# Optimization experiments

Hardware: AMD Instinct MI355X
Metric: run time of the kernel (lower is better)

## Reference

```python
import jax, jax.numpy as jnp
import numpy as np

DIM = 2048
N_HEADS = 16
N_KV_HEADS = 4
HEAD_DIM = DIM // N_HEADS


def setup_inputs() -> dict:
    key = jax.random.key(0)
    k1, k2, k3, k4, k5 = jax.random.split(key, 5)
    B, T = 2, 2048
    scale = 1.0 / np.sqrt(DIM)
    x = jax.random.normal(k1, (B, T, DIM), dtype=jnp.float32)
    # weights stored as [in, out] so forward is x @ W (same math as nn.Linear)
    Wq = jax.random.normal(k2, (DIM, DIM), dtype=jnp.float32) * scale
    Wk = jax.random.normal(k3, (DIM, N_KV_HEADS * HEAD_DIM), dtype=jnp.float32) * scale
    Wv = jax.random.normal(k4, (DIM, N_KV_HEADS * HEAD_DIM), dtype=jnp.float32) * scale
    Wo = jax.random.normal(k5, (DIM, DIM), dtype=jnp.float32) * scale
    return {"x": x, "Wq": Wq, "Wk": Wk, "Wv": Wv, "Wo": Wo}


def reference(x, Wq, Wk, Wv, Wo):
    B, T, C = x.shape
    G = N_HEADS // N_KV_HEADS  # query heads per kv head
    # projections
    q = (x @ Wq).reshape(B, T, N_KV_HEADS, G, HEAD_DIM)   # [B,T,K,G,d]
    k = (x @ Wk).reshape(B, T, N_KV_HEADS, HEAD_DIM)      # [B,T,K,d]
    v = (x @ Wv).reshape(B, T, N_KV_HEADS, HEAD_DIM)      # [B,T,K,d]
    # attention scores: grouped heads share kv head (no repeat_interleave copy)
    att = jnp.einsum('btkgd,bskd->bkgts', q, k) / np.sqrt(HEAD_DIM)  # [B,K,G,T,T]
    att = jax.nn.softmax(att, axis=-1)
    out = jnp.einsum('bkgts,bskd->btkgd', att, v).reshape(B, T, C)
    return out @ Wo
```

## Files before the change

kernel.cpp:

```cpp
#include <hip/hip_runtime.h>
#include <hip/hip_bf16.h>

typedef __hip_bfloat16 bf16;
typedef __attribute__((ext_vector_type(8))) short short8;
typedef __attribute__((ext_vector_type(4))) short short4v;
typedef __attribute__((ext_vector_type(4))) float f32x4;

#define DIMC 2048
#define TSEQ 2048
#define NB 2
#define KVH 4
#define NH 16
#define HD 128
#define KVD 512
#define QSCALE 0.12751744f

#if __has_builtin(__builtin_amdgcn_exp2f)
#define EXP2(x) __builtin_amdgcn_exp2f(x)
#else
#define EXP2(x) exp2f(x)
#endif

__device__ __forceinline__ void mfma16(f32x4& acc, short8 a, short8 b) {
  acc = __builtin_amdgcn_mfma_f32_16x16x32_bf16(a, b, acc, 0, 0, 0);
}

__device__ __forceinline__ void gload_lds16(const bf16* g, bf16* l) {
  __builtin_amdgcn_global_load_lds(
      (const __attribute__((address_space(1))) void*)g,
      (__attribute__((address_space(3))) void*)l, 16, 0, 0);
}

__device__ __forceinline__ int swz(int row, int col) {
  return col ^ ((row & 7) << 3);
}

__global__ __launch_bounds__(256) void f2b(const float* __restrict__ in,
                                           bf16* __restrict__ out, long n4) {
  long i = (long)blockIdx.x * 256 + threadIdx.x;
  if (i >= n4) return;
  const f32x4 v = *(const f32x4*)(in + i * 4);
  union { short4v s; bf16 h[4]; } u;
#pragma unroll
  for (int j = 0; j < 4; ++j) u.h[j] = __float2bfloat16(v[j]);
  *(short4v*)(out + i * 4) = u.s;
}

__global__ __launch_bounds__(256) void transpose_all(const float* __restrict__ Wq,
                                                     const float* __restrict__ Wk,
                                                     const float* __restrict__ Wv,
                                                     const float* __restrict__ Wo,
                                                     bf16* __restrict__ WT3,
                                                     bf16* __restrict__ WoT) {
  __shared__ bf16 tile[64][72];
  const int y = blockIdx.y;
  const float* in;
  bf16* out;
  int C, rb, cb;
  float scale = 1.0f;
  if (y < 32) {
    in = Wq; out = WT3; C = 2048;
    rb = y * 64; cb = blockIdx.x * 64; scale = QSCALE;
  } else if (y < 40) {
    in = Wk; out = WT3 + (long)2048 * DIMC; C = 512;
    rb = blockIdx.x * 64; cb = (y - 32) * 64;
  } else if (y < 48) {
    in = Wv; out = WT3 + (long)2560 * DIMC; C = 512;
    rb = blockIdx.x * 64; cb = (y - 40) * 64;
  } else {
    in = Wo; out = WoT; C = 2048;
    rb = (y - 48) * 64; cb = blockIdx.x * 64;
  }
  int tx = threadIdx.x & 63, ty = threadIdx.x >> 6;
  for (int i = ty; i < 64; i += 4)
    tile[i][tx] = __float2bfloat16(in[(long)(rb + i) * C + cb + tx] * scale);
  __syncthreads();
  for (int i = ty; i < 64; i += 4)
    out[(long)(cb + i) * DIMC + rb + tx] = tile[tx][i];
}

#define GEMM_BODY(A_, Bt_, K_)                                                  \
  const int tid = threadIdx.x;                                                  \
  const int lane = tid & 63, wid = tid >> 6;                                    \
  const long m0 = blockIdx.y * 128, n0 = blockIdx.x * 128;                      \
  const int wm = (wid >> 1) * 64, wn = (wid & 1) * 64;                          \
  f32x4 acc[4][4] = {};                                                         \
  const int srow = lane >> 2, scol = (lane & 3) * 8;                            \
  const bf16* Ag = A_ + (m0 + srow) * (long)K_ + scol;                          \
  const bf16* Bg = Bt_ + (n0 + srow) * (long)K_ + scol;                         \
  for (int k0 = 0; k0 < K_; k0 += 32) {                                         \
    for (int p = 0; p < 2; ++p) {                                               \
      int rr = p * 64 + wid * 16;                                               \
      gload_lds16(Ag + (long)rr * K_ + k0, As + rr * 32);                       \
      gload_lds16(Bg + (long)rr * K_ + k0, Bs + rr * 32);                       \
    }                                                                           \
    __syncthreads();                                                            \
    const int ko = (lane >> 4) * 8;                                             \
    short8 af[4], bq[4];                                                        \
    _Pragma("unroll") for (int i = 0; i < 4; ++i) {                             \
      af[i] = *(const short8*)(As + (wm + i * 16 + (lane & 15)) * 32 + ko);     \
      bq[i] = *(const short8*)(Bs + (wn + i * 16 + (lane & 15)) * 32 + ko);     \
    }                                                                           \
    _Pragma("unroll") for (int i = 0; i < 4; ++i)                               \
      _Pragma("unroll") for (int j = 0; j < 4; ++j)                             \
        mfma16(acc[i][j], af[i], bq[j]);                                        \
    __syncthreads();                                                            \
  }                                                                             \
  const int cr = (lane >> 4) * 4, cc = lane & 15;

__global__ __launch_bounds__(256) void gemm_qkv(const bf16* __restrict__ A,
                                                const bf16* __restrict__ Bt,
                                                bf16* __restrict__ qp,
                                                bf16* __restrict__ kp,
                                                bf16* __restrict__ vT) {
  __shared__ bf16 As[128 * 32];
  __shared__ bf16 Bs[128 * 32];
  GEMM_BODY(A, Bt, 2048)
#pragma unroll
  for (int i = 0; i < 4; ++i)
#pragma unroll
    for (int j = 0; j < 4; ++j)
#pragma unroll
      for (int r = 0; r < 4; ++r) {
        long m = m0 + wm + i * 16 + cr + r;
        long n = n0 + wn + j * 16 + cc;
        float val = acc[i][j][r];
        if (n0 < 2048) {
          qp[m * DIMC + n] = __float2bfloat16(val);
        } else if (n0 < 2560) {
          kp[m * KVD + (n - 2048)] = __float2bfloat16(val);
        } else {
          long nn = n - 2560;
          long z = (m >> 11) * 4 + (nn >> 7);
          vT[z * (HD * (long)TSEQ) + (nn & 127) * (long)TSEQ + (m & 2047)] =
              __float2bfloat16(val);
        }
      }
}

__global__ __launch_bounds__(256) void gemm_out(const bf16* __restrict__ A,
                                                const bf16* __restrict__ Bt,
                                                float* __restrict__ C) {
  __shared__ bf16 As[128 * 32];
  __shared__ bf16 Bs[128 * 32];
  GEMM_BODY(A, Bt, 2048)
#pragma unroll
  for (int i = 0; i < 4; ++i)
#pragma unroll
    for (int j = 0; j < 4; ++j)
#pragma unroll
      for (int r = 0; r < 4; ++r) {
        long m = m0 + wm + i * 16 + cr + r;
        long n = n0 + wn + j * 16 + cc;
        C[m * DIMC + n] = acc[i][j][r];
      }
}

__global__ __launch_bounds__(256, 2) void attn_fwd(const bf16* __restrict__ Qp,
                                                   const bf16* __restrict__ Kp,
                                                   const bf16* __restrict__ Vt,
                                                   bf16* __restrict__ op2,
                                                   float* __restrict__ mlb) {
  __shared__ bf16 Ks[2][32 * 128];
  __shared__ bf16 Vts[2][128 * 32];
  const int tid = threadIdx.x;
  const int lane = tid & 63, wid = tid >> 6;
  const int h = blockIdx.y;
  const int z = blockIdx.z;
  const int b = z & 1, half = z >> 1;
  const int s_lo = half * 1024, s_hi = s_lo + 1024;
  const int kv = h >> 2;
  const int t0 = blockIdx.x * 128;
  const int lr = lane & 15, lg = lane >> 4;

  short8 aq[2][4];
#pragma unroll
  for (int f = 0; f < 2; ++f) {
    const bf16* qrow =
        Qp + ((long)(b * TSEQ + t0 + wid * 32 + f * 16 + lr)) * DIMC + h * HD + lg * 8;
#pragma unroll
    for (int c = 0; c < 4; ++c) aq[f][c] = *(const short8*)(qrow + c * 32);
  }
  f32x4 o[2][8] = {};
  float mrun[2] = {-1e30f, -1e30f}, lrun[2] = {0.f, 0.f};

  const bf16* Kg = Kp + (long)b * TSEQ * KVD + kv * HD;
  const bf16* Vg = Vt + ((long)(b * KVH + kv)) * HD * TSEQ;

  const int krow = tid >> 3, kc0 = (tid & 7) * 16;
  const int vrow = tid >> 1, va = tid & 1;
  short8 kreg[2], vreg[2];
#pragma unroll
  for (int p = 0; p < 2; ++p) {
    kreg[p] = *(const short8*)(Kg + (long)(s_lo + krow) * KVD + kc0 + p * 8);
    vreg[p] = *(const short8*)(Vg + (long)vrow * TSEQ + s_lo + va * 16 + 8 * p);
  }

  for (int s0 = s_lo; s0 < s_hi; s0 += 32) {
    const int buf = (s0 >> 5) & 1;
    bf16* Kb = Ks[buf];
    bf16* Vb = Vts[buf];
#pragma unroll
    for (int p = 0; p < 2; ++p) {
      *(short8*)(Kb + krow * 128 + swz(krow, kc0 + p * 8)) = kreg[p];
      union { short8 v8; short4v q[2]; } u;
      u.v8 = vreg[p];
      int q1 = (2 * p + vrow) & 3, q2 = (2 * p + 1 + vrow) & 3;
      *(short4v*)(Vb + vrow * 32 + q1 * 8 + va * 4) = u.q[0];
      *(short4v*)(Vb + vrow * 32 + q2 * 8 + va * 4) = u.q[1];
    }
    __syncthreads();
    if (s0 + 32 < s_hi) {
#pragma unroll
      for (int p = 0; p < 2; ++p) {
        kreg[p] = *(const short8*)(Kg + (long)(s0 + 32 + krow) * KVD + kc0 + p * 8);
        vreg[p] = *(const short8*)(Vg + (long)vrow * TSEQ + s0 + 32 + va * 16 + 8 * p);
      }
    }

    f32x4 sacc[2][2] = {};
    __builtin_amdgcn_s_setprio(1);
#pragma unroll
    for (int sf = 0; sf < 2; ++sf)
#pragma unroll
      for (int c = 0; c < 4; ++c) {
        int row = sf * 16 + lr;
        short8 kf = *(const short8*)(Kb + row * 128 + swz(row, c * 32 + lg * 8));
        mfma16(sacc[0][sf], kf, aq[0][c]);
        mfma16(sacc[1][sf], kf, aq[1][c]);
      }
    __builtin_amdgcn_s_setprio(0);

    union { short8 s; bf16 h[8]; } pb[2];
#pragma unroll
    for (int f = 0; f < 2; ++f) {
      float tmax = sacc[f][0][0];
#pragma unroll
      for (int sf = 0; sf < 2; ++sf)
#pragma unroll
        for (int r = 0; r < 4; ++r) tmax = fmaxf(tmax, sacc[f][sf][r]);
      tmax = fmaxf(tmax, __shfl_xor(tmax, 16));
      tmax = fmaxf(tmax, __shfl_xor(tmax, 32));
      if (__any(tmax > mrun[f] + 8.0f)) {
        float mnew = fmaxf(mrun[f], tmax);
        float fac = EXP2(mrun[f] - mnew);
        mrun[f] = mnew;
        lrun[f] *= fac;
#pragma unroll
        for (int df = 0; df < 8; ++df) o[f][df] *= fac;
      }
      float ps = 0.f;
#pragma unroll
      for (int r = 0; r < 4; ++r) {
        float v0 = EXP2(sacc[f][0][r] - mrun[f]);
        float v1 = EXP2(sacc[f][1][r] - mrun[f]);
        ps += v0 + v1;
        pb[f].h[r] = __float2bfloat16(v0);
        pb[f].h[4 + r] = __float2bfloat16(v1);
      }
      ps += __shfl_xor(ps, 16);
      ps += __shfl_xor(ps, 32);
      lrun[f] += ps;
    }

    __builtin_amdgcn_s_setprio(1);
#pragma unroll
    for (int df = 0; df < 8; ++df) {
      int row = df * 16 + lr;
      short8 vf = *(const short8*)(Vb + row * 32 + ((lg + row) & 3) * 8);
      mfma16(o[0][df], vf, pb[0].s);
      mfma16(o[1][df], vf, pb[1].s);
    }
    __builtin_amdgcn_s_setprio(0);
  }

#pragma unroll
  for (int f = 0; f < 2; ++f) {
    int t = t0 + wid * 32 + f * 16 + lr;
    bf16* obase = op2 + ((long)z * TSEQ + t) * DIMC + h * HD + lg * 4;
#pragma unroll
    for (int df = 0; df < 8; ++df) {
      union { short4v s; bf16 h[4]; } ov;
#pragma unroll
      for (int r = 0; r < 4; ++r) ov.h[r] = __float2bfloat16(o[f][df][r]);
      *(short4v*)(obase + df * 16) = ov.s;
    }
    if (lg == 0) {
      long mi = ((long)z * TSEQ + t) * NH + h;
      mlb[mi] = mrun[f];
      mlb[(long)4 * TSEQ * NH + mi] = lrun[f];
    }
  }
}

__global__ __launch_bounds__(256) void attn_combine(bf16* __restrict__ op2,
                                                    const float* __restrict__ mlb) {
  long idx = (long)blockIdx.x * 256 + threadIdx.x;
  int r = idx >> 8, c8 = idx & 255;
  int b = r >> 11, t = r & 2047, h = c8 >> 4;
  long z1 = b, z2 = 2 + b;
  long m1i = (z1 * TSEQ + t) * NH + h, m2i = (z2 * TSEQ + t) * NH + h;
  const long loff = (long)4 * TSEQ * NH;
  float m1 = mlb[m1i], m2 = mlb[m2i];
  float l1 = mlb[loff + m1i], l2 = mlb[loff + m2i];
  float m = fmaxf(m1, m2);
  float a1 = EXP2(m1 - m), a2 = EXP2(m2 - m);
  float inv = 1.0f / (l1 * a1 + l2 * a2);
  a1 *= inv; a2 *= inv;
  union { short8 s; bf16 h[8]; } o1, o2, ov;
  o1.s = *(const short8*)(op2 + (z1 * TSEQ + t) * DIMC + c8 * 8);
  o2.s = *(const short8*)(op2 + (z2 * TSEQ + t) * DIMC + c8 * 8);
#pragma unroll
  for (int j = 0; j < 8; ++j)
    ov.h[j] = __float2bfloat16(__bfloat162float(o1.h[j]) * a1 +
                               __bfloat162float(o2.h[j]) * a2);
  *(short8*)(op2 + (z1 * TSEQ + t) * DIMC + c8 * 8) = ov.s;
}

extern "C" void kernel_launch(void* const* d_in, const int* in_sizes, int n_in,
                              void* d_out, int out_size, void* d_ws, size_t ws_size,
                              hipStream_t stream) {
  const float* x  = (const float*)d_in[0];
  const float* Wq = (const float*)d_in[1];
  const float* Wk = (const float*)d_in[2];
  const float* Wv = (const float*)d_in[3];
  const float* Wo = (const float*)d_in[4];
  float* out = (float*)d_out;
  bf16* ws = (bf16*)d_ws;

  bf16* xb    = ws;
  bf16* WT3   = xb + 8388608;
  bf16* spare = WT3 + 6291456;
  bf16* WoT   = spare + 2097152;
  bf16* qp    = WoT + 4194304;
  bf16* kp    = qp + 8388608;
  bf16* vT    = kp + 2097152;
  float* mlb  = (float*)(vT + 2097152);
  bf16* op2   = xb;
  bf16* ao    = op2;

  f2b<<<8192, 256, 0, stream>>>(x, xb, 2097152);
  transpose_all<<<dim3(32, 80), 256, 0, stream>>>(Wq, Wk, Wv, Wo, WT3, WoT);

  gemm_qkv<<<dim3(24, 32), 256, 0, stream>>>(xb, WT3, qp, kp, vT);

  attn_fwd<<<dim3(16, 16, 4), 256, 0, stream>>>(qp, kp, vT, op2, mlb);
  attn_combine<<<4096, 256, 0, stream>>>(op2, mlb);

  gemm_out<<<dim3(16, 32), 256, 0, stream>>>(ao, WoT, out);
}
```

Before: 248.4 us.

## Widen attention KV tile to 64 keys with single LDS buffer

The attention kernel now processes 64 keys per iteration instead of 32, halving the number of loop iterations, softmax max/sum reductions and shuffles per key. The double-buffered LDS is replaced by a single 64-key buffer with a trailing barrier, and the V layout swizzle is widened to 8 slots. The register prefetch of the next tile is kept. This adds a second __syncthreads per iteration and more live registers (sacc, prefetch regs), which may affect occupancy at 2 blocks per SIMD.

```diff
diff --git a/kernel.cpp b/kernel.cpp
--- a/kernel.cpp
+++ b/kernel.cpp
@@ -161,8 +161,8 @@
                                                    const bf16* __restrict__ Vt,
                                                    bf16* __restrict__ op2,
                                                    float* __restrict__ mlb) {
-  __shared__ bf16 Ks[2][32 * 128];
-  __shared__ bf16 Vts[2][128 * 32];
+  __shared__ bf16 Ks[64 * 128];
+  __shared__ bf16 Vts[128 * 64];
   const int tid = threadIdx.x;
   const int lane = tid & 63, wid = tid >> 6;
   const int h = blockIdx.y;
@@ -187,56 +187,65 @@
   const bf16* Kg = Kp + (long)b * TSEQ * KVD + kv * HD;
   const bf16* Vg = Vt + ((long)(b * KVH + kv)) * HD * TSEQ;
 
-  const int krow = tid >> 3, kc0 = (tid & 7) * 16;
-  const int vrow = tid >> 1, va = tid & 1;
-  short8 kreg[2], vreg[2];
-#pragma unroll
-  for (int p = 0; p < 2; ++p) {
-    kreg[p] = *(const short8*)(Kg + (long)(s_lo + krow) * KVD + kc0 + p * 8);
-    vreg[p] = *(const short8*)(Vg + (long)vrow * TSEQ + s_lo + va * 16 + 8 * p);
-  }
-
-  for (int s0 = s_lo; s0 < s_hi; s0 += 32) {
-    const int buf = (s0 >> 5) & 1;
-    bf16* Kb = Ks[buf];
-    bf16* Vb = Vts[buf];
+  const int krow = tid >> 2;
+  const int vrow = tid >> 1;
+  short8 kreg[2][2], vreg[2][2];
+#pragma unroll
+  for (int s = 0; s < 2; ++s)
 #pragma unroll
     for (int p = 0; p < 2; ++p) {
-      *(short8*)(Kb + krow * 128 + swz(krow, kc0 + p * 8)) = kreg[p];
-      union { short8 v8; short4v q[2]; } u;
-      u.v8 = vreg[p];
-      int q1 = (2 * p + vrow) & 3, q2 = (2 * p + 1 + vrow) & 3;
-      *(short4v*)(Vb + vrow * 32 + q1 * 8 + va * 4) = u.q[0];
-      *(short4v*)(Vb + vrow * 32 + q2 * 8 + va * 4) = u.q[1];
-    }
+      kreg[s][p] = *(const short8*)(Kg + (long)(s_lo + krow) * KVD + (2 * (tid & 3) + s) * 16 + p * 8);
+      vreg[s][p] = *(const short8*)(Vg + (long)vrow * TSEQ + s_lo + (2 * (tid & 1) + s) * 16 + 8 * p);
+    }
+
+  for (int s0 = s_lo; s0 < s_hi; s0 += 64) {
+#pragma unroll
+    for (int s = 0; s < 2; ++s)
+#pragma unroll
+      for (int p = 0; p < 2; ++p) {
+        int kc0 = (2 * (tid & 3) + s) * 16;
+        *(short8*)(Ks + krow * 128 + swz(krow, kc0 + p * 8)) = kreg[s][p];
+        int va = 2 * (tid & 1) + s;
+        union { short8 v8; short4v q[2]; } u;
+        u.v8 = vreg[s][p];
+        int sl1 = (4 * (va >> 1) + 2 * p + vrow) & 7;
+        int sl2 = (4 * (va >> 1) + 2 * p + 1 + vrow) & 7;
+        int hf = (va & 1) * 4;
+        *(short4v*)(Vts + vrow * 64 + sl1 * 8 + hf) = u.q[0];
+        *(short4v*)(Vts + vrow * 64 + sl2 * 8 + hf) = u.q[1];
+      }
     __syncthreads();
-    if (s0 + 32 < s_hi) {
-#pragma unroll
-      for (int p = 0; p < 2; ++p) {
-        kreg[p] = *(const short8*)(Kg + (long)(s0 + 32 + krow) * KVD + kc0 + p * 8);
-        vreg[p] = *(const short8*)(Vg + (long)vrow * TSEQ + s0 + 32 + va * 16 + 8 * p);
-      }
-    }
-
-    f32x4 sacc[2][2] = {};
+    if (s0 + 64 < s_hi) {
+#pragma unroll
+      for (int s = 0; s < 2; ++s)
+#pragma unroll
+        for (int p = 0; p < 2; ++p) {
+          kreg[s][p] = *(const short8*)(Kg + (long)(s0 + 64 + krow) * KVD +
+                                        (2 * (tid & 3) + s) * 16 + p * 8);
+          vreg[s][p] = *(const short8*)(Vg + (long)vrow * TSEQ + s0 + 64 +
+                                        (2 * (tid & 1) + s) * 16 + 8 * p);
+        }
+    }
+
+    f32x4 sacc[2][4] = {};
     __builtin_amdgcn_s_setprio(1);
 #pragma unroll
-    for (int sf = 0; sf < 2; ++sf)
+    for (int sf = 0; sf < 4; ++sf)
 #pragma unroll
       for (int c = 0; c < 4; ++c) {
         int row = sf * 16 + lr;
-        short8 kf = *(const short8*)(Kb + row * 128 + swz(row, c * 32 + lg * 8));
+        short8 kf = *(const short8*)(Ks + row * 128 + swz(row, c * 32 + lg * 8));
         mfma16(sacc[0][sf], kf, aq[0][c]);
         mfma16(sacc[1][sf], kf, aq[1][c]);
       }
     __builtin_amdgcn_s_setprio(0);
 
-    union { short8 s; bf16 h[8]; } pb[2];
+    union { short8 s; bf16 h[8]; } pb[2][2];
 #pragma unroll
     for (int f = 0; f < 2; ++f) {
       float tmax = sacc[f][0][0];
 #pragma unroll
-      for (int sf = 0; sf < 2; ++sf)
+      for (int sf = 0; sf < 4; ++sf)
 #pragma unroll
         for (int r = 0; r < 4; ++r) tmax = fmaxf(tmax, sacc[f][sf][r]);
       tmax = fmaxf(tmax, __shfl_xor(tmax, 16));
@@ -249,29 +258,41 @@
 #pragma unroll
         for (int df = 0; df < 8; ++df) o[f][df] *= fac;
       }
+      float p4[4][4];
       float ps = 0.f;
 #pragma unroll
-      for (int r = 0; r < 4; ++r) {
-        float v0 = EXP2(sacc[f][0][r] - mrun[f]);
-        float v1 = EXP2(sacc[f][1][r] - mrun[f]);
-        ps += v0 + v1;
-        pb[f].h[r] = __float2bfloat16(v0);
-        pb[f].h[4 + r] = __float2bfloat16(v1);
-      }
+      for (int sf = 0; sf < 4; ++sf)
+#pragma unroll
+        for (int r = 0; r < 4; ++r) {
+          float pv = EXP2(sacc[f][sf][r] - mrun[f]);
+          p4[sf][r] = pv;
+          ps += pv;
+        }
       ps += __shfl_xor(ps, 16);
       ps += __shfl_xor(ps, 32);
       lrun[f] += ps;
+#pragma unroll
+      for (int c2 = 0; c2 < 2; ++c2)
+#pragma unroll
+        for (int r = 0; r < 4; ++r) {
+          pb[f][c2].h[r] = __float2bfloat16(p4[2 * c2][r]);
+          pb[f][c2].h[4 + r] = __float2bfloat16(p4[2 * c2 + 1][r]);
+        }
     }
 
     __builtin_amdgcn_s_setprio(1);
 #pragma unroll
-    for (int df = 0; df < 8; ++df) {
-      int row = df * 16 + lr;
-      short8 vf = *(const short8*)(Vb + row * 32 + ((lg + row) & 3) * 8);
-      mfma16(o[0][df], vf, pb[0].s);
-      mfma16(o[1][df], vf, pb[1].s);
+    for (int c2 = 0; c2 < 2; ++c2) {
+#pragma unroll
+      for (int df = 0; df < 8; ++df) {
+        int row = df * 16 + lr;
+        short8 vf = *(const short8*)(Vts + row * 64 + ((4 * c2 + lg + row) & 7) * 8);
+        mfma16(o[0][df], vf, pb[0][c2].s);
+        mfma16(o[1][df], vf, pb[1][c2].s);
+      }
     }
     __builtin_amdgcn_s_setprio(0);
+    __syncthreads();
   }
 
 #pragma unroll
```

Measured after the change: 241.9 us. 2.6% less time.
